# Performance work log

Hardware: AMD Instinct MI355X
Metric: run time of the kernel (lower is better)

Reference implementation:

```python
import jax, jax.numpy as jnp
import numpy as np

V, E, H, H2, T, B, S = 50000, 300, 512, 256, 10, 64, 256
START_IDX, STOP_IDX = 8, 9


def setup_inputs() -> dict:
    key = jax.random.key(0)
    ks = jax.random.split(key, 16)
    sd = 1.0 / np.sqrt(H2)
    inp = {
        'sentence': jax.random.randint(ks[0], (B, S), 0, V, dtype=jnp.int32),
        'emb': jax.random.normal(ks[1], (V, E), jnp.float32),
        'wih_f': jax.random.uniform(ks[2], (4 * H2, E), jnp.float32, -sd, sd),
        'whh_f': jax.random.uniform(ks[3], (4 * H2, H2), jnp.float32, -sd, sd),
        'bih_f': jax.random.uniform(ks[4], (4 * H2,), jnp.float32, -sd, sd),
        'bhh_f': jax.random.uniform(ks[5], (4 * H2,), jnp.float32, -sd, sd),
        'wih_b': jax.random.uniform(ks[6], (4 * H2, E), jnp.float32, -sd, sd),
        'whh_b': jax.random.uniform(ks[7], (4 * H2, H2), jnp.float32, -sd, sd),
        'bih_b': jax.random.uniform(ks[8], (4 * H2,), jnp.float32, -sd, sd),
        'bhh_b': jax.random.uniform(ks[9], (4 * H2,), jnp.float32, -sd, sd),
        'W_out': jax.random.uniform(ks[10], (T, H), jnp.float32, -1.0 / np.sqrt(H), 1.0 / np.sqrt(H)),
        'b_out': jax.random.uniform(ks[11], (T,), jnp.float32, -1.0 / np.sqrt(H), 1.0 / np.sqrt(H)),
        'h0': jax.random.normal(ks[12], (2, B, H2), jnp.float32),
        'c0': jax.random.normal(ks[13], (2, B, H2), jnp.float32),
    }
    trans = jax.random.normal(ks[14], (T, T), jnp.float32)
    trans = trans.at[START_IDX, :].set(-10000.0).at[:, STOP_IDX].set(-10000.0)
    inp['transitions'] = trans
    return inp


def _lstm_dir(x, h0, c0, wih, whh, bih, bhh, reverse):
    # x: (S, B, E); returns hidden states (S, B, H2)
    def step(carry, xt):
        h, c = carry
        g = xt @ wih.T + bih + h @ whh.T + bhh  # (B, 4*H2)
        i, f, gg, o = jnp.split(g, 4, axis=-1)  # PyTorch gate order i,f,g,o
        c = jax.nn.sigmoid(f) * c + jax.nn.sigmoid(i) * jnp.tanh(gg)
        h = jax.nn.sigmoid(o) * jnp.tanh(c)
        return (h, c), h
    _, hs = jax.lax.scan(step, (h0, c0), x, reverse=reverse)
    return hs


def _features(sentence, emb, wih_f, whh_f, bih_f, bhh_f, wih_b, whh_b, bih_b, bhh_b,
              W_out, b_out, h0, c0):
    # Replicate torch's .view(seq,batch,-1): raw memory reinterpretation of (B,S,E)
    embeds = emb[sentence].reshape(S, B, E)
    h_f = _lstm_dir(embeds, h0[0], c0[0], wih_f, whh_f, bih_f, bhh_f, False)
    h_b = _lstm_dir(embeds, h0[1], c0[1], wih_b, whh_b, bih_b, bhh_b, True)
    lstm_out = jnp.concatenate([h_f, h_b], axis=-1)  # (S, B, H)
    # Replicate torch's .view(batch,-1,hidden): reinterpretation, not transpose
    lstm_out = lstm_out.reshape(B, S, H)
    return lstm_out @ W_out.T + b_out  # (B, S, T)


def _viterbi(feats, transitions):
    # feats: (B, S, T)
    init = jnp.full((B, T), -10000.0, feats.dtype).at[:, START_IDX].set(0.0)

    def step(fv, feat_t):
        # ntv[b, next, prev] = fv[b, prev] + transitions[next, prev]
        ntv = fv[:, None, :] + transitions[None, :, :]
        vv = jnp.max(ntv, axis=2)          # (B, T)
        bp = jnp.argmax(ntv, axis=2)       # (B, T) backpointers
        return vv + feat_t, bp

    fv, bps = jax.lax.scan(step, init, jnp.swapaxes(feats, 0, 1))  # bps: (S, B, T)
    terminal = fv + transitions[STOP_IDX]
    path_score = jnp.max(terminal, axis=1)[:, None]   # (B, 1)
    last_tag = jnp.argmax(terminal, axis=1)           # (B,)

    def back(best, bp):
        return bp[jnp.arange(B), best], best

    _, path = jax.lax.scan(back, last_tag, bps, reverse=True)  # (S, B)
    return path_score, path.T  # (B, 1), (B, S)


def reference(sentence, emb, wih_f, whh_f, bih_f, bhh_f, wih_b, whh_b, bih_b, bhh_b,
              W_out, b_out, transitions, h0, c0):
    feats = _features(sentence, emb, wih_f, whh_f, bih_f, bhh_f,
                      wih_b, whh_b, bih_b, bhh_b, W_out, b_out, h0, c0)
    return _viterbi(feats, transitions)
```

## Files before the change

kernel.cpp:

```cpp
#include <hip/hip_runtime.h>

#define E_    300
#define H2_   256
#define B_    64
#define S_    256
#define G_    (S_*B_)
#define GATES (4*H2_)
#define NS    8

__global__ void prep_kernel(const float* __restrict__ whh_f, const float* __restrict__ whh_b,
                            const float* __restrict__ bih_f, const float* __restrict__ bhh_f,
                            const float* __restrict__ bih_b, const float* __restrict__ bhh_b,
                            float* __restrict__ wpack, float* __restrict__ bsum) {
    int idx = blockIdx.x * blockDim.x + threadIdx.x;
    if (idx < 2 * 8 * 512 * 64) {
        int d  = idx >> 18;
        int s  = (idx >> 15) & 7;
        int t  = (idx >> 6) & 511;
        int e  = idx & 63;
        int gt = e >> 4, kk = e & 15;
        int u  = t >> 4, cc = t & 15;
        int row = gt * 256 + s * 32 + u;
        int col = cc * 16 + kk;
        const float* w = d ? whh_b : whh_f;
        wpack[idx] = w[row * H2_ + col];
    }
    if (idx < 2 * GATES) {
        int d = idx >> 10, j = idx & 1023;
        bsum[idx] = d ? (bih_b[j] + bhh_b[j]) : (bih_f[j] + bhh_f[j]);
    }
}

__global__ __launch_bounds__(256) void xproj_kernel(
    const int* __restrict__ sent, const float* __restrict__ emb,
    const float* __restrict__ wih_f, const float* __restrict__ wih_b,
    const float* __restrict__ bsum, float* __restrict__ xp) {
    __shared__ float As[128 * 21];
    __shared__ float Bs[20 * 64];
    __shared__ int   toks[128];
    int gt = blockIdx.x, jt = blockIdx.y, d = blockIdx.z;
    const float* wih = d ? wih_b : wih_f;
    int tid = threadIdx.x;
    int g0 = gt * 128, j0 = jt * 64;
    if (tid < 128) toks[tid] = sent[g0 + tid];
    __syncthreads();

    int ty = tid >> 4, tx = tid & 15;
    float acc[8][4];
    float4 bv = *(const float4*)&bsum[d * 1024 + j0 + tx * 4];
    #pragma unroll
    for (int i = 0; i < 8; i++) { acc[i][0] = bv.x; acc[i][1] = bv.y; acc[i][2] = bv.z; acc[i][3] = bv.w; }

    for (int kt = 0; kt < 15; kt++) {
        int k0 = kt * 20;
        #pragma unroll
        for (int l = 0; l < 10; l++) {
            int e = l * 256 + tid; int i = e / 20, k = e % 20;
            As[i * 21 + k] = emb[(long)toks[i] * E_ + k0 + k];
        }
        #pragma unroll
        for (int l = 0; l < 5; l++) {
            int e = l * 256 + tid; int k = e >> 6, j = e & 63;
            Bs[k * 64 + j] = wih[(j0 + j) * E_ + k0 + k];
        }
        __syncthreads();
        #pragma unroll
        for (int k = 0; k < 20; k++) {
            float4 b4 = *(const float4*)&Bs[k * 64 + tx * 4];
            #pragma unroll
            for (int i = 0; i < 8; i++) {
                float a = As[(ty * 8 + i) * 21 + k];
                acc[i][0] += a * b4.x; acc[i][1] += a * b4.y;
                acc[i][2] += a * b4.z; acc[i][3] += a * b4.w;
            }
        }
        __syncthreads();
    }
    #pragma unroll
    for (int i = 0; i < 8; i++) {
        float4 o; o.x = acc[i][0]; o.y = acc[i][1]; o.z = acc[i][2]; o.w = acc[i][3];
        *(float4*)&xp[((long)d * G_ + g0 + ty * 8 + i) * 1024 + j0 + tx * 4] = o;
    }
}

__global__ __launch_bounds__(512, 2) void lstm_kernel(
    const float* __restrict__ xp, const float* __restrict__ wpack,
    const float* __restrict__ h0, const float* __restrict__ c0,
    float* __restrict__ hcat, unsigned long long* __restrict__ mbox) {
    __shared__ float h_cur[4 * 320];
    __shared__ float part[4 * 2180];

    int t = threadIdx.x;
    int bid = blockIdx.x;
    int x = bid & 7, rest = bid >> 3;
    int s = rest & 7, Ghi = rest >> 3;
    int G = Ghi * 8 + x;
    int d = G >> 4, bg = G & 15;

    float4 w[4][4];
    const float4* wbase = (const float4*)(wpack + (size_t)((d * 8 + s) * 512 + t) * 64);
    #pragma unroll
    for (int gt = 0; gt < 4; gt++)
        #pragma unroll
        for (int k4 = 0; k4 < 4; k4++)
            w[gt][k4] = wbase[gt * 4 + k4];

    int fu = t >> 4, fcc = t & 15;
    int rgt = t & 3, ru = t >> 2;

    for (int e = t; e < 1024; e += 512) {
        int j = e >> 8, k = e & 255;
        h_cur[j * 320 + (k >> 4) * 20 + (k & 15)] = h0[(d * B_ + bg * 4 + j) * H2_ + k];
    }
    float c[4] = {0.f, 0.f, 0.f, 0.f};
    if (t < 128 && rgt == 0) {
        #pragma unroll
        for (int j = 0; j < 4; j++)
            c[j] = c0[(d * B_ + bg * 4 + j) * H2_ + s * 32 + ru];
    }
    unsigned long long* mb_out = mbox + (size_t)(G * NS + s) * 256;
    const size_t xbase = (size_t)d * G_ * 1024;
    __syncthreads();

    for (int step = 0; step < S_; step++) {
        int sidx = d ? (255 - step) : step;
        float xv[4] = {0.f, 0.f, 0.f, 0.f};
        if (t < 128) {
            #pragma unroll
            for (int j = 0; j < 4; j++)
                xv[j] = xp[xbase + (size_t)(sidx * 64 + bg * 4 + j) * 1024
                           + rgt * 256 + s * 32 + ru];
        }
        float acc[4][4];
        #pragma unroll
        for (int gt = 0; gt < 4; gt++)
            #pragma unroll
            for (int j = 0; j < 4; j++) acc[gt][j] = 0.f;
        #pragma unroll
        for (int j = 0; j < 4; j++) {
            const float* hb = &h_cur[j * 320 + fcc * 20];
            #pragma unroll
            for (int k4 = 0; k4 < 4; k4++) {
                float4 h4 = *(const float4*)(hb + k4 * 4);
                #pragma unroll
                for (int gt = 0; gt < 4; gt++) {
                    acc[gt][j] += w[gt][k4].x * h4.x + w[gt][k4].y * h4.y
                                + w[gt][k4].z * h4.z + w[gt][k4].w * h4.w;
                }
            }
        }
        #pragma unroll
        for (int gt = 0; gt < 4; gt++) {
            float4 p; p.x = acc[gt][0]; p.y = acc[gt][1]; p.z = acc[gt][2]; p.w = acc[gt][3];
            *(float4*)&part[gt * 2180 + fu * 68 + fcc * 4] = p;
        }
        __syncthreads();

        if (t < 128) {
            float4 sum; sum.x = xv[0]; sum.y = xv[1]; sum.z = xv[2]; sum.w = xv[3];
            #pragma unroll
            for (int cc = 0; cc < 16; cc++) {
                float4 p = *(const float4*)&part[rgt * 2180 + ru * 68 + cc * 4];
                sum.x += p.x; sum.y += p.y; sum.z += p.z; sum.w += p.w;
            }
            int lb = t & ~3;
            float gi[4], gf[4], gg[4], go[4];
            #pragma unroll
            for (int j = 0; j < 4; j++) {
                float v = (&sum.x)[j];
                gi[j] = __shfl(v, lb + 0);
                gf[j] = __shfl(v, lb + 1);
                gg[j] = __shfl(v, lb + 2);
                go[j] = __shfl(v, lb + 3);
            }
            if (rgt == 0) {
                int u = ru, k = s * 32 + u;
                #pragma unroll
                for (int j = 0; j < 4; j++) {
                    float si = 1.f / (1.f + __expf(-gi[j]));
                    float sf = 1.f / (1.f + __expf(-gf[j]));
                    float so = 1.f / (1.f + __expf(-go[j]));
                    float tg = tanhf(gg[j]);
                    c[j] = sf * c[j] + si * tg;
                    float h = so * tanhf(c[j]);
                    h_cur[j * 320 + (k >> 4) * 20 + (k & 15)] = h;
                    union { float f; unsigned u32; } cv; cv.f = h;
                    __hip_atomic_store(&mb_out[(step & 1) * 128 + j * 32 + u],
                        ((unsigned long long)(unsigned)(step + 1) << 32) | cv.u32,
                        __ATOMIC_RELAXED, __HIP_MEMORY_SCOPE_AGENT);
                    hcat[(size_t)(sidx * 64 + bg * 4 + j) * 512 + d * 256 + k] = h;
                }
            }
        } else {
            int pt = t - 128;
            #pragma unroll
            for (int r = 0; r < 3; r++) {
                int vv = pt + r * 384;
                if (vv < 896) {
                    int spr = vv >> 7;
                    int sp = spr + (spr >= s ? 1 : 0);
                    int rem = vv & 127;
                    int j = rem >> 5, u = rem & 31;
                    unsigned long long* ad =
                        mbox + (size_t)(G * NS + sp) * 256 + (step & 1) * 128 + rem;
                    unsigned long long val;
                    do {
                        val = __hip_atomic_load(ad, __ATOMIC_RELAXED, __HIP_MEMORY_SCOPE_AGENT);
                    } while ((unsigned)(val >> 32) != (unsigned)(step + 1));
                    union { unsigned u32; float f; } cv; cv.u32 = (unsigned)val;
                    int k = sp * 32 + u;
                    h_cur[j * 320 + (k >> 4) * 20 + (k & 15)] = cv.f;
                }
            }
        }
        __syncthreads();
    }
}

__global__ void feats_kernel(const float* __restrict__ hcat, const float* __restrict__ Wout,
                             const float* __restrict__ bout, float* __restrict__ feats) {
    int tid = threadIdx.x; int w = tid >> 6, l = tid & 63;
    int g = blockIdx.x * 4 + w;
    float r[8];
    #pragma unroll
    for (int m = 0; m < 8; m++) r[m] = hcat[(long)g * 512 + m * 64 + l];
    #pragma unroll
    for (int tt = 0; tt < 10; tt++) {
        float a = 0.f;
        #pragma unroll
        for (int m = 0; m < 8; m++) a += r[m] * Wout[tt * 512 + m * 64 + l];
        #pragma unroll
        for (int off = 32; off > 0; off >>= 1) a += __shfl_down(a, off);
        if (l == 0) feats[g * 10 + tt] = a + bout[tt];
    }
}

__global__ void viterbi_kernel(const float* __restrict__ feats, const float* __restrict__ trans,
                               float* __restrict__ out) {
    __shared__ unsigned char bp[256 * 16];
    int l = threadIdx.x; int b = blockIdx.x;
    float trrow[10];
    #pragma unroll
    for (int p = 0; p < 10; p++) trrow[p] = (l < 10) ? trans[l * 10 + p] : 0.f;
    float tr_stop = (l < 10) ? trans[90 + l] : -3e38f;
    float fv = (l == 8) ? 0.f : -10000.f;

    for (int s = 0; s < 256; s++) {
        float m = -3e38f; int arg = 0;
        #pragma unroll
        for (int p = 0; p < 10; p++) {
            float v = __shfl(fv, p) + trrow[p];
            if (v > m) { m = v; arg = p; }
        }
        float ft = (l < 10) ? feats[((long)b * 256 + s) * 10 + l] : 0.f;
        fv = m + ft;
        if (l < 10) bp[s * 16 + l] = (unsigned char)arg;
    }
    __syncthreads();
    float term = fv + tr_stop;
    float best = -3e38f; int bt = 0;
    #pragma unroll
    for (int p = 0; p < 10; p++) {
        float v = __shfl(term, p);
        if (v > best) { best = v; bt = p; }
    }
    if (l == 0) {
        out[b] = best;
        int cur = bt;
        out[64 + b * 256 + 255] = (float)cur;
        for (int s = 254; s >= 0; s--) {
            cur = bp[(s + 1) * 16 + cur];
            out[64 + b * 256 + s] = (float)cur;
        }
    }
}

extern "C" void kernel_launch(void* const* d_in, const int* in_sizes, int n_in,
                              void* d_out, int out_size, void* d_ws, size_t ws_size,
                              hipStream_t stream) {
    const int*   sent  = (const int*)  d_in[0];
    const float* emb   = (const float*)d_in[1];
    const float* wih_f = (const float*)d_in[2];
    const float* whh_f = (const float*)d_in[3];
    const float* bih_f = (const float*)d_in[4];
    const float* bhh_f = (const float*)d_in[5];
    const float* wih_b = (const float*)d_in[6];
    const float* whh_b = (const float*)d_in[7];
    const float* bih_b = (const float*)d_in[8];
    const float* bhh_b = (const float*)d_in[9];
    const float* Wout  = (const float*)d_in[10];
    const float* bout  = (const float*)d_in[11];
    const float* h0    = (const float*)d_in[12];
    const float* c0    = (const float*)d_in[13];
    const float* trans = (const float*)d_in[14];

    float* ws    = (float*)d_ws;
    float* xp    = ws;
    float* hcat  = ws + 33554432;
    float* wpack = ws + 41943040;
    float* bsum  = ws + 42467328;
    unsigned long long* mbox = (unsigned long long*)(ws + 42469376);
    float* feats = ws;
    float* out   = (float*)d_out;

    hipLaunchKernelGGL(prep_kernel, dim3(2048), dim3(256), 0, stream,
                       whh_f, whh_b, bih_f, bhh_f, bih_b, bhh_b, wpack, bsum);
    hipLaunchKernelGGL(xproj_kernel, dim3(128, 16, 2), dim3(256), 0, stream,
                       sent, emb, wih_f, wih_b, bsum, xp);

    void* lstm_args[] = { (void*)&xp, (void*)&wpack, (void*)&h0, (void*)&c0,
                          (void*)&hcat, (void*)&mbox };
    hipLaunchCooperativeKernel((const void*)lstm_kernel, dim3(256), dim3(512),
                               lstm_args, 0, stream);

    hipLaunchKernelGGL(feats_kernel, dim3(4096), dim3(256), 0, stream,
                       hcat, Wout, bout, feats);
    hipLaunchKernelGGL(viterbi_kernel, dim3(64), dim3(64), 0, stream,
                       feats, trans, out);
}
```

Measured before the change: 1.454 ms.

## Replace LDS partial-sum reduction with butterfly shuffle transpose-reduce in LSTM step

The per-step gate partial sums are now reduced across the 16 k-slice lanes with a register butterfly of xor shuffles, instead of being written to a shared `part` buffer and summed by 128 threads. Each lane ends up holding one gate/batch value. Gate activations are then spread over 128 lanes, one batch element each, and the mailbox polling is spread over all threads. The shared array is enlarged to 21760 floats, which likely limits the kernel to one block per CU. This trades shared-memory traffic and a serial summation for extra shuffle instructions, and the larger allocation could change occupancy or residency assumptions for the spin-wait.

```diff
diff --git a/kernel.cpp b/kernel.cpp
--- a/kernel.cpp
+++ b/kernel.cpp
@@ -87,8 +87,7 @@
     const float* __restrict__ xp, const float* __restrict__ wpack,
     const float* __restrict__ h0, const float* __restrict__ c0,
     float* __restrict__ hcat, unsigned long long* __restrict__ mbox) {
-    __shared__ float h_cur[4 * 320];
-    __shared__ float part[4 * 2180];
+    __shared__ float h_cur[21760];
 
     int t = threadIdx.x;
     int bid = blockIdx.x;
@@ -96,6 +95,8 @@
     int s = rest & 7, Ghi = rest >> 3;
     int G = Ghi * 8 + x;
     int d = G >> 4, bg = G & 15;
+    int u = t >> 4, cc = t & 15;
+    int gt_m = cc >> 2, j_m = cc & 3;
 
     float4 w[4][4];
     const float4* wbase = (const float4*)(wpack + (size_t)((d * 8 + s) * 512 + t) * 64);
@@ -104,33 +105,23 @@
         #pragma unroll
         for (int k4 = 0; k4 < 4; k4++)
             w[gt][k4] = wbase[gt * 4 + k4];
-
-    int fu = t >> 4, fcc = t & 15;
-    int rgt = t & 3, ru = t >> 2;
 
     for (int e = t; e < 1024; e += 512) {
         int j = e >> 8, k = e & 255;
         h_cur[j * 320 + (k >> 4) * 20 + (k & 15)] = h0[(d * B_ + bg * 4 + j) * H2_ + k];
     }
-    float c[4] = {0.f, 0.f, 0.f, 0.f};
-    if (t < 128 && rgt == 0) {
-        #pragma unroll
-        for (int j = 0; j < 4; j++)
-            c[j] = c0[(d * B_ + bg * 4 + j) * H2_ + s * 32 + ru];
-    }
+    float c = 0.f;
+    if (cc < 4) c = c0[(d * B_ + bg * 4 + cc) * H2_ + s * 32 + u];
+
     unsigned long long* mb_out = mbox + (size_t)(G * NS + s) * 256;
     const size_t xbase = (size_t)d * G_ * 1024;
     __syncthreads();
 
     for (int step = 0; step < S_; step++) {
         int sidx = d ? (255 - step) : step;
-        float xv[4] = {0.f, 0.f, 0.f, 0.f};
-        if (t < 128) {
-            #pragma unroll
-            for (int j = 0; j < 4; j++)
-                xv[j] = xp[xbase + (size_t)(sidx * 64 + bg * 4 + j) * 1024
-                           + rgt * 256 + s * 32 + ru];
-        }
+        float xv = xp[xbase + (size_t)(sidx * 64 + bg * 4 + j_m) * 1024
+                      + gt_m * 256 + s * 32 + u];
+
         float acc[4][4];
         #pragma unroll
         for (int gt = 0; gt < 4; gt++)
@@ -138,7 +129,7 @@
             for (int j = 0; j < 4; j++) acc[gt][j] = 0.f;
         #pragma unroll
         for (int j = 0; j < 4; j++) {
-            const float* hb = &h_cur[j * 320 + fcc * 20];
+            const float* hb = &h_cur[j * 320 + cc * 20];
             #pragma unroll
             for (int k4 = 0; k4 < 4; k4++) {
                 float4 h4 = *(const float4*)(hb + k4 * 4);
@@ -149,69 +140,70 @@
                 }
             }
         }
-        #pragma unroll
-        for (int gt = 0; gt < 4; gt++) {
-            float4 p; p.x = acc[gt][0]; p.y = acc[gt][1]; p.z = acc[gt][2]; p.w = acc[gt][3];
-            *(float4*)&part[gt * 2180 + fu * 68 + fcc * 4] = p;
-        }
         __syncthreads();
 
-        if (t < 128) {
-            float4 sum; sum.x = xv[0]; sum.y = xv[1]; sum.z = xv[2]; sum.w = xv[3];
+        float a_[16];
+        #pragma unroll
+        for (int gt = 0; gt < 4; gt++)
             #pragma unroll
-            for (int cc = 0; cc < 16; cc++) {
-                float4 p = *(const float4*)&part[rgt * 2180 + ru * 68 + cc * 4];
-                sum.x += p.x; sum.y += p.y; sum.z += p.z; sum.w += p.w;
-            }
-            int lb = t & ~3;
-            float gi[4], gf[4], gg[4], go[4];
-            #pragma unroll
-            for (int j = 0; j < 4; j++) {
-                float v = (&sum.x)[j];
-                gi[j] = __shfl(v, lb + 0);
-                gf[j] = __shfl(v, lb + 1);
-                gg[j] = __shfl(v, lb + 2);
-                go[j] = __shfl(v, lb + 3);
-            }
-            if (rgt == 0) {
-                int u = ru, k = s * 32 + u;
-                #pragma unroll
-                for (int j = 0; j < 4; j++) {
-                    float si = 1.f / (1.f + __expf(-gi[j]));
-                    float sf = 1.f / (1.f + __expf(-gf[j]));
-                    float so = 1.f / (1.f + __expf(-go[j]));
-                    float tg = tanhf(gg[j]);
-                    c[j] = sf * c[j] + si * tg;
-                    float h = so * tanhf(c[j]);
-                    h_cur[j * 320 + (k >> 4) * 20 + (k & 15)] = h;
-                    union { float f; unsigned u32; } cv; cv.f = h;
-                    __hip_atomic_store(&mb_out[(step & 1) * 128 + j * 32 + u],
-                        ((unsigned long long)(unsigned)(step + 1) << 32) | cv.u32,
-                        __ATOMIC_RELAXED, __HIP_MEMORY_SCOPE_AGENT);
-                    hcat[(size_t)(sidx * 64 + bg * 4 + j) * 512 + d * 256 + k] = h;
-                }
-            }
-        } else {
-            int pt = t - 128;
-            #pragma unroll
-            for (int r = 0; r < 3; r++) {
-                int vv = pt + r * 384;
-                if (vv < 896) {
-                    int spr = vv >> 7;
-                    int sp = spr + (spr >= s ? 1 : 0);
-                    int rem = vv & 127;
-                    int j = rem >> 5, u = rem & 31;
-                    unsigned long long* ad =
-                        mbox + (size_t)(G * NS + sp) * 256 + (step & 1) * 128 + rem;
-                    unsigned long long val;
-                    do {
-                        val = __hip_atomic_load(ad, __ATOMIC_RELAXED, __HIP_MEMORY_SCOPE_AGENT);
-                    } while ((unsigned)(val >> 32) != (unsigned)(step + 1));
-                    union { unsigned u32; float f; } cv; cv.u32 = (unsigned)val;
-                    int k = sp * 32 + u;
-                    h_cur[j * 320 + (k >> 4) * 20 + (k & 15)] = cv.f;
-                }
-            }
+            for (int j = 0; j < 4; j++) a_[gt * 4 + j] = acc[gt][j];
+        bool p0 = (cc & 1), p1 = (cc & 2), p2 = (cc & 4), p3 = (cc & 8);
+        float b_[8];
+        #pragma unroll
+        for (int m = 0; m < 8; m++) {
+            float lo = a_[2 * m], hi = a_[2 * m + 1];
+            b_[m] = (p0 ? hi : lo) + __shfl_xor(p0 ? lo : hi, 1);
+        }
+        float c_[4];
+        #pragma unroll
+        for (int m = 0; m < 4; m++) {
+            float lo = b_[2 * m], hi = b_[2 * m + 1];
+            c_[m] = (p1 ? hi : lo) + __shfl_xor(p1 ? lo : hi, 2);
+        }
+        float d_[2];
+        #pragma unroll
+        for (int m = 0; m < 2; m++) {
+            float lo = c_[2 * m], hi = c_[2 * m + 1];
+            d_[m] = (p2 ? hi : lo) + __shfl_xor(p2 ? lo : hi, 4);
+        }
+        float ev = (p3 ? d_[1] : d_[0]) + __shfl_xor(p3 ? d_[0] : d_[1], 8);
+        ev += xv;
+
+        int base = t & ~15;
+        float fv = __shfl(ev, base + 4 + (t & 3));
+        float gv = __shfl(ev, base + 8 + (t & 3));
+        float ov = __shfl(ev, base + 12 + (t & 3));
+
+        if (cc < 4) {
+            float si = 1.f / (1.f + __expf(-ev));
+            float sf = 1.f / (1.f + __expf(-fv));
+            float so = 1.f / (1.f + __expf(-ov));
+            float tg = tanhf(gv);
+            c = sf * c + si * tg;
+            float h = so * tanhf(c);
+            int k = s * 32 + u;
+            h_cur[cc * 320 + (k >> 4) * 20 + (k & 15)] = h;
+            union { float f; unsigned u32; } cv; cv.f = h;
+            __hip_atomic_store(&mb_out[(step & 1) * 128 + cc * 32 + u],
+                ((unsigned long long)(unsigned)(step + 1) << 32) | cv.u32,
+                __ATOMIC_RELAXED, __HIP_MEMORY_SCOPE_AGENT);
+            hcat[(size_t)(sidx * 64 + bg * 4 + cc) * 512 + d * 256 + k] = h;
+        }
+
+        for (int vv = t; vv < 896; vv += 512) {
+            int spr = vv >> 7;
+            int sp = spr + (spr >= s ? 1 : 0);
+            int rem = vv & 127;
+            int j = rem >> 5, uu = rem & 31;
+            unsigned long long* ad =
+                mbox + (size_t)(G * NS + sp) * 256 + (step & 1) * 128 + rem;
+            unsigned long long val;
+            do {
+                val = __hip_atomic_load(ad, __ATOMIC_RELAXED, __HIP_MEMORY_SCOPE_AGENT);
+            } while ((unsigned)(val >> 32) != (unsigned)(step + 1));
+            union { unsigned u32; float f; } cv; cv.u32 = (unsigned)val;
+            int k = sp * 32 + uu;
+            h_cur[j * 320 + (k >> 4) * 20 + (k & 15)] = cv.f;
         }
         __syncthreads();
     }
```

Measured after the change: 1.671 ms. +14.9%, slower.
